# Optimization experiments

Hardware: AMD Instinct MI355X
Metric: run time of the kernel (lower is better)

Reference implementation:

```python
import jax, jax.numpy as jnp
import numpy as np

NUM_HEADS = 16
HEAD_DIM = 64
INNER = NUM_HEADS * HEAD_DIM  # 1024
QUERY_DIM = 1024
CONTEXT_DIM = 768
SCALE = HEAD_DIM ** -0.5


def setup_inputs() -> dict:
    key = jax.random.key(0)
    ks = jax.random.split(key, 6)
    B, NQ, NKV = 8, 1024, 2048
    query = jax.random.normal(ks[0], (B, NQ, QUERY_DIM), dtype=jnp.float32)
    context = jax.random.normal(ks[1], (B, NKV, CONTEXT_DIM), dtype=jnp.float32)
    # weights stored as [in, out] (transpose of torch Linear), math-equivalent
    w_q = jax.random.normal(ks[2], (QUERY_DIM, INNER), dtype=jnp.float32) * (QUERY_DIM ** -0.5)
    w_kv = jax.random.normal(ks[3], (CONTEXT_DIM, 2 * INNER), dtype=jnp.float32) * (CONTEXT_DIM ** -0.5)
    w_out = jax.random.normal(ks[4], (INNER, QUERY_DIM), dtype=jnp.float32) * (INNER ** -0.5)
    b_out = jax.random.normal(ks[5], (QUERY_DIM,), dtype=jnp.float32) * 0.01
    return {"query": query, "context": context, "w_q": w_q, "w_kv": w_kv,
            "w_out": w_out, "b_out": b_out}


def reference(query, context, w_q, w_kv, w_out, b_out):
    B, NQ, _ = query.shape
    NKV = context.shape[1]
    q = query @ w_q                              # [B, NQ, INNER]
    kv = context @ w_kv                          # [B, NKV, 2*INNER]
    k, v = jnp.split(kv, 2, axis=-1)
    # reshape to [B, H, N, D]
    q = q.reshape(B, NQ, NUM_HEADS, HEAD_DIM).transpose(0, 2, 1, 3)
    k = k.reshape(B, NKV, NUM_HEADS, HEAD_DIM).transpose(0, 2, 1, 3)
    v = v.reshape(B, NKV, NUM_HEADS, HEAD_DIM).transpose(0, 2, 1, 3)
    scores = jnp.einsum('bhqd,bhkd->bhqk', q, k) * SCALE
    attn = jax.nn.softmax(scores, axis=-1)
    out = jnp.einsum('bhqk,bhkd->bhqd', attn, v)  # [B, H, NQ, D]
    out = out.transpose(0, 2, 1, 3).reshape(B, NQ, INNER)
    return out @ w_out + b_out
```

## Files before the change

kernel.cpp:

```cpp
#include <hip/hip_runtime.h>
#include <stdint.h>

typedef __bf16 bf16_t;
typedef bf16_t bf16x8 __attribute__((ext_vector_type(8)));
typedef float f32x4 __attribute__((ext_vector_type(4)));
typedef float f32x16 __attribute__((ext_vector_type(16)));

__device__ __forceinline__ unsigned short f2bf(float x) {
    unsigned u = __builtin_bit_cast(unsigned, x);
    u = (u + 0x7FFFu + ((u >> 16) & 1u)) >> 16;
    return (unsigned short)u;
}

__device__ __forceinline__ unsigned pk_bf16(float lo, float hi) {
    unsigned u0 = __builtin_bit_cast(unsigned, lo) + 0x8000u;
    unsigned u1 = __builtin_bit_cast(unsigned, hi) + 0x8000u;
    return __builtin_amdgcn_perm(u1, u0, 0x07060302u);
}

__device__ __forceinline__ void async_load16(const void* g, void* lds) {
    auto* gp = reinterpret_cast<const __attribute__((address_space(1))) uint32_t*>(
        reinterpret_cast<uintptr_t>(g));
    auto* lp = reinterpret_cast<__attribute__((address_space(3))) uint32_t*>(
        reinterpret_cast<uintptr_t>(lds));
    __builtin_amdgcn_global_load_lds(gp, lp, 16, 0, 0);
}

__global__ __launch_bounds__(256) void cast_f32_bf16(const float* __restrict__ src,
                                                     unsigned short* __restrict__ dst,
                                                     int n8) {
    int i = blockIdx.x * 256 + threadIdx.x;
    if (i >= n8) return;
    const float4* s4 = (const float4*)src;
    float4 a = s4[i * 2], b = s4[i * 2 + 1];
    uint4 o;
    o.x = (unsigned)f2bf(a.x) | ((unsigned)f2bf(a.y) << 16);
    o.y = (unsigned)f2bf(a.z) | ((unsigned)f2bf(a.w) << 16);
    o.z = (unsigned)f2bf(b.x) | ((unsigned)f2bf(b.y) << 16);
    o.w = (unsigned)f2bf(b.z) | ((unsigned)f2bf(b.w) << 16);
    ((uint4*)dst)[i] = o;
}

__global__ __launch_bounds__(256) void transcast(const float* __restrict__ src,
                                                 unsigned short* __restrict__ dst,
                                                 int K, int N, float scale) {
    __shared__ float tile[32][33];
    int x = threadIdx.x, y = threadIdx.y;
    int c0 = blockIdx.x * 32, r0 = blockIdx.y * 32;
    #pragma unroll
    for (int i = 0; i < 32; i += 8)
        tile[y + i][x] = src[(size_t)(r0 + y + i) * N + c0 + x];
    __syncthreads();
    #pragma unroll
    for (int i = 0; i < 32; i += 8)
        dst[(size_t)(c0 + y + i) * K + r0 + x] = f2bf(tile[x][y + i] * scale);
}

template <int EPI>
__global__ __launch_bounds__(256) void gemm_bt(const unsigned short* __restrict__ A,
                                               const unsigned short* __restrict__ Bt,
                                               void* __restrict__ Cout,
                                               const float* __restrict__ bias,
                                               int K, int N, int nkt) {
    __shared__ __align__(16) unsigned short lA[128 * 64];
    __shared__ __align__(16) unsigned short lB[128 * 64];
    const int tid = threadIdx.x;
    const int w = tid >> 6, l = tid & 63;
    const int wm = w >> 1, wn = w & 1;
    const int row0 = blockIdx.y * 128, col0 = blockIdx.x * 128;
    const int lrow = l & 15, lq = l >> 4;
    const int srow = l >> 3;
    const int scol = ((l & 7) ^ srow) * 8;

    f32x4 acc[4][4];
    #pragma unroll
    for (int i = 0; i < 4; ++i)
        #pragma unroll
        for (int j = 0; j < 4; ++j) acc[i][j] = (f32x4)0.f;

    for (int kt = 0; kt < nkt; ++kt) {
        const int k0 = kt * 64;
        __syncthreads();
        #pragma unroll
        for (int q = 0; q < 4; ++q) {
            int r = (w * 4 + q) * 8 + srow;
            async_load16(A + (size_t)(row0 + r) * K + k0 + scol,
                         (char*)lA + (w * 4 + q) * 1024);
            async_load16(Bt + (size_t)(col0 + r) * K + k0 + scol,
                         (char*)lB + (w * 4 + q) * 1024);
        }
        __syncthreads();
        #pragma unroll
        for (int kc = 0; kc < 2; ++kc) {
            const int pc = ((kc * 4 + lq) ^ (lrow & 7)) * 16;
            bf16x8 af[4], bfr[4];
            #pragma unroll
            for (int i = 0; i < 4; ++i)
                af[i] = *(const bf16x8*)((const char*)lA + (wm * 64 + i * 16 + lrow) * 128 + pc);
            #pragma unroll
            for (int j = 0; j < 4; ++j)
                bfr[j] = *(const bf16x8*)((const char*)lB + (wn * 64 + j * 16 + lrow) * 128 + pc);
            #pragma unroll
            for (int i = 0; i < 4; ++i)
                #pragma unroll
                for (int j = 0; j < 4; ++j)
                    acc[i][j] = __builtin_amdgcn_mfma_f32_16x16x32_bf16(af[i], bfr[j],
                                                                        acc[i][j], 0, 0, 0);
        }
    }
    #pragma unroll
    for (int i = 0; i < 4; ++i) {
        const int grow0 = row0 + wm * 64 + i * 16 + lq * 4;
        #pragma unroll
        for (int j = 0; j < 4; ++j) {
            const int gcol = col0 + wn * 64 + j * 16 + lrow;
            #pragma unroll
            for (int r = 0; r < 4; ++r) {
                float v = acc[i][j][r];
                int grow = grow0 + r;
                if (EPI == 0) {
                    ((unsigned short*)Cout)[(size_t)grow * N + gcol] = f2bf(v);
                } else {
                    ((float*)Cout)[(size_t)grow * N + gcol] = v + bias[gcol];
                }
            }
        }
    }
}

__global__ __launch_bounds__(256, 2) void gemm_kv(const unsigned short* __restrict__ A,
                                                  const unsigned short* __restrict__ Bt,
                                                  unsigned short* __restrict__ Kb,
                                                  unsigned short* __restrict__ Vt) {
    __shared__ __align__(16) unsigned short lA[256 * 64];
    __shared__ __align__(16) unsigned short lB[128 * 64];
    const int tid = threadIdx.x;
    const int w = tid >> 6, l = tid & 63;
    const int wm = w >> 1, wn = w & 1;
    const int row0 = blockIdx.y * 256, col0 = blockIdx.x * 128;
    const int r32 = l & 31, hw = l >> 5;
    const int srow = l >> 3, scol = ((l & 7) ^ srow) * 8;

    f32x16 acc[4][2];
    #pragma unroll
    for (int mi = 0; mi < 4; ++mi)
        #pragma unroll
        for (int ni = 0; ni < 2; ++ni) acc[mi][ni] = (f32x16)0.f;

    const unsigned short* ga = A + (size_t)(row0 + w * 8 + srow) * 768 + scol;
    const unsigned short* gb = Bt + (size_t)(col0 + w * 8 + srow) * 768 + scol;
    char* lAw = (char*)lA + (w * 8) * 128;
    char* lBw = (char*)lB + (w * 8) * 128;
    const char* lap = (const char*)lA + (wm * 128 + r32) * 128;
    const char* lbp = (const char*)lB + (wn * 64 + r32) * 128;
    const int r7 = r32 & 7;

    for (int kt = 0; kt < 12; ++kt) {
        __syncthreads();
        #pragma unroll
        for (int q = 0; q < 8; ++q)
            async_load16(ga + (size_t)q * 32 * 768, lAw + q * 32 * 128);
        #pragma unroll
        for (int q = 0; q < 4; ++q)
            async_load16(gb + (size_t)q * 32 * 768, lBw + q * 32 * 128);
        ga += 64;
        gb += 64;
        __syncthreads();
        #pragma unroll
        for (int ks = 0; ks < 4; ++ks) {
            const int off = ((ks * 2 + hw) ^ r7) * 16;
            bf16x8 af[4], bfr[2];
            #pragma unroll
            for (int mi = 0; mi < 4; ++mi)
                af[mi] = *(const bf16x8*)(lap + mi * 32 * 128 + off);
            #pragma unroll
            for (int ni = 0; ni < 2; ++ni)
                bfr[ni] = *(const bf16x8*)(lbp + ni * 32 * 128 + off);
            #pragma unroll
            for (int mi = 0; mi < 4; ++mi)
                #pragma unroll
                for (int ni = 0; ni < 2; ++ni)
                    acc[mi][ni] = __builtin_amdgcn_mfma_f32_32x32x16_bf16(af[mi], bfr[ni],
                                                                          acc[mi][ni], 0, 0, 0);
        }
    }

    if (col0 < 1024) {
        unsigned short* kp = Kb + (size_t)(row0 + wm * 128) * 1024 + col0 + wn * 64 + r32;
        #pragma unroll
        for (int mi = 0; mi < 4; ++mi)
            #pragma unroll
            for (int ni = 0; ni < 2; ++ni)
                #pragma unroll
                for (int reg = 0; reg < 16; ++reg) {
                    int rr = mi * 32 + (reg & 3) + 8 * (reg >> 2) + 4 * hw;
                    kp[(size_t)rr * 1024 + ni * 32] = f2bf(acc[mi][ni][reg]);
                }
    } else {
        const int bb = row0 >> 11;
        const int keybase = (row0 & 2047) + wm * 128 + 4 * hw;
        const int fvbase = col0 - 1024 + wn * 64 + r32;
        unsigned short* vp = Vt + ((size_t)bb * 1024 + fvbase) * 2048 + keybase;
        #pragma unroll
        for (int mi = 0; mi < 4; ++mi)
            #pragma unroll
            for (int ni = 0; ni < 2; ++ni)
                #pragma unroll
                for (int g = 0; g < 4; ++g) {
                    uint2 pk2;
                    pk2.x = pk_bf16(acc[mi][ni][g * 4 + 0], acc[mi][ni][g * 4 + 1]);
                    pk2.y = pk_bf16(acc[mi][ni][g * 4 + 2], acc[mi][ni][g * 4 + 3]);
                    *(uint2*)(vp + (size_t)(ni * 32) * 2048 + mi * 32 + g * 8) = pk2;
                }
    }
}

__global__ __launch_bounds__(256, 4) void attn_fwd(const unsigned short* __restrict__ qb,
                                                   const unsigned short* __restrict__ kb,
                                                   const unsigned short* __restrict__ vt,
                                                   unsigned short* __restrict__ ob) {
    constexpr int PSTR = 72;
    __shared__ __align__(16) unsigned short lK[64 * 64];
    __shared__ __align__(16) unsigned short lV[64 * 64];
    __shared__ __align__(16) unsigned short lP[4][32 * PSTR];
    const int tid = threadIdx.x;
    const int w = tid >> 6, l = tid & 63;
    const int b = blockIdx.z, h = blockIdx.y, q0 = blockIdx.x * 128;
    const int lrow = l & 15, lq = l >> 4;
    const int srow = l >> 3, scol = ((l & 7) ^ (srow & 7)) * 8;

    bf16x8 bq[2][2];
    #pragma unroll
    for (int qs = 0; qs < 2; ++qs)
        #pragma unroll
        for (int kc = 0; kc < 2; ++kc) {
            int row = b * 1024 + q0 + w * 32 + qs * 16 + lrow;
            int col = h * 64 + kc * 32 + lq * 8;
            bq[qs][kc] = *(const bf16x8*)(qb + (size_t)row * 1024 + col);
        }

    f32x4 ot[2][4];
    f32x4 lsv[2];
    #pragma unroll
    for (int qs = 0; qs < 2; ++qs) {
        #pragma unroll
        for (int dt = 0; dt < 4; ++dt) ot[qs][dt] = (f32x4)0.f;
        lsv[qs] = (f32x4)0.f;
    }

    const char* kp0 = (const char*)lK + lrow * 128 + ((lq ^ (lrow & 7)) * 16);
    const char* kp1 = (const char*)lK + lrow * 128 + (((4 + lq) ^ (lrow & 7)) * 16);
    const char* vp0 = (const char*)lV + lrow * 128 + ((lq ^ (lrow & 7)) * 16);
    const char* vp1 = (const char*)lV + lrow * 128 + (((4 + lq) ^ (lrow & 7)) * 16);
    char* pw[2];
    const char* pr[2];
    #pragma unroll
    for (int qs = 0; qs < 2; ++qs) {
        pw[qs] = (char*)&lP[w][(qs * 16 + lrow) * PSTR + 4 * lq];
        pr[qs] = (const char*)&lP[w][(qs * 16 + lrow) * PSTR + 8 * lq];
    }

    const unsigned short* gkp = kb + (size_t)b * 2048 * 1024 + h * 64 +
                                (size_t)(w * 8 + srow) * 1024 + scol;
    const unsigned short* gvp = vt + (size_t)(b * 1024 + h * 64) * 2048 +
                                (size_t)(w * 8 + srow) * 2048 + scol;
    char* lKw0 = (char*)lK + (w * 8) * 128;
    char* lKw1 = (char*)lK + (32 + w * 8) * 128;
    char* lVw0 = (char*)lV + (w * 8) * 128;
    char* lVw1 = (char*)lV + (32 + w * 8) * 128;

    for (int it = 0; it < 32; ++it) {
        __syncthreads();
        async_load16(gkp, lKw0);
        async_load16(gkp + 32 * 1024, lKw1);
        async_load16(gvp, lVw0);
        async_load16(gvp + 32 * 2048, lVw1);
        gkp += 64 * 1024;
        gvp += 64;
        __syncthreads();

        f32x4 st[2][4];
        #pragma unroll
        for (int mt = 0; mt < 4; ++mt) {
            bf16x8 ka0 = *(const bf16x8*)(kp0 + mt * 2048);
            bf16x8 ka1 = *(const bf16x8*)(kp1 + mt * 2048);
            #pragma unroll
            for (int qs = 0; qs < 2; ++qs) {
                f32x4 c = (f32x4)0.f;
                c = __builtin_amdgcn_mfma_f32_16x16x32_bf16(ka0, bq[qs][0], c, 0, 0, 0);
                c = __builtin_amdgcn_mfma_f32_16x16x32_bf16(ka1, bq[qs][1], c, 0, 0, 0);
                st[qs][mt] = c;
            }
        }

        #pragma unroll
        for (int qs = 0; qs < 2; ++qs) {
            #pragma unroll
            for (int mt = 0; mt < 4; ++mt)
                #pragma unroll
                for (int r = 0; r < 4; ++r)
                    st[qs][mt][r] = __builtin_amdgcn_exp2f(st[qs][mt][r]);
            lsv[qs] += (st[qs][0] + st[qs][1]) + (st[qs][2] + st[qs][3]);
            #pragma unroll
            for (int mt = 0; mt < 4; ++mt) {
                uint2 pk;
                pk.x = pk_bf16(st[qs][mt][0], st[qs][mt][1]);
                pk.y = pk_bf16(st[qs][mt][2], st[qs][mt][3]);
                *(uint2*)(pw[qs] + 32 * mt) = pk;
            }
        }

        bf16x8 pb[2][2];
        #pragma unroll
        for (int qs = 0; qs < 2; ++qs)
            #pragma unroll
            for (int kcg = 0; kcg < 2; ++kcg)
                pb[qs][kcg] = *(const bf16x8*)(pr[qs] + 64 * kcg);

        #pragma unroll
        for (int dt = 0; dt < 4; ++dt) {
            bf16x8 va0 = *(const bf16x8*)(vp0 + dt * 2048);
            bf16x8 va1 = *(const bf16x8*)(vp1 + dt * 2048);
            #pragma unroll
            for (int qs = 0; qs < 2; ++qs) {
                ot[qs][dt] = __builtin_amdgcn_mfma_f32_16x16x32_bf16(va0, pb[qs][0], ot[qs][dt], 0, 0, 0);
                ot[qs][dt] = __builtin_amdgcn_mfma_f32_16x16x32_bf16(va1, pb[qs][1], ot[qs][dt], 0, 0, 0);
            }
        }
    }

    #pragma unroll
    for (int qs = 0; qs < 2; ++qs) {
        float rs = (lsv[qs][0] + lsv[qs][1]) + (lsv[qs][2] + lsv[qs][3]);
        rs += __shfl_xor(rs, 16);
        rs += __shfl_xor(rs, 32);
        float inv = 1.f / rs;
        size_t grow = (size_t)(b * 1024 + q0 + w * 32 + qs * 16 + lrow);
        unsigned short* op = ob + grow * 1024 + h * 64 + 4 * lq;
        #pragma unroll
        for (int dt = 0; dt < 4; ++dt) {
            uint2 pk;
            pk.x = pk_bf16(ot[qs][dt][0] * inv, ot[qs][dt][1] * inv);
            pk.y = pk_bf16(ot[qs][dt][2] * inv, ot[qs][dt][3] * inv);
            *(uint2*)(op + 16 * dt) = pk;
        }
    }
}

extern "C" void kernel_launch(void* const* d_in, const int* in_sizes, int n_in,
                              void* d_out, int out_size, void* d_ws, size_t ws_size,
                              hipStream_t stream) {
    const float* query   = (const float*)d_in[0];
    const float* context = (const float*)d_in[1];
    const float* w_q     = (const float*)d_in[2];
    const float* w_kv    = (const float*)d_in[3];
    const float* w_out   = (const float*)d_in[4];
    const float* b_out   = (const float*)d_in[5];
    float* out = (float*)d_out;

    char* p = (char*)d_ws;
    unsigned short* qin   = (unsigned short*)p; p += (size_t)8192 * 1024 * 2;
    unsigned short* cin   = (unsigned short*)p; p += (size_t)16384 * 768 * 2;
    unsigned short* wqT   = (unsigned short*)p; p += (size_t)1024 * 1024 * 2;
    unsigned short* wkvT  = (unsigned short*)p; p += (size_t)2048 * 768 * 2;
    unsigned short* woutT = (unsigned short*)p; p += (size_t)1024 * 1024 * 2;
    unsigned short* qproj = (unsigned short*)p; p += (size_t)8192 * 1024 * 2;
    unsigned short* kbuf  = (unsigned short*)p; p += (size_t)16384 * 1024 * 2;
    unsigned short* vT    = (unsigned short*)p; p += (size_t)16384 * 1024 * 2;
    unsigned short* obuf  = (unsigned short*)p; p += (size_t)8192 * 1024 * 2;

    const float qscale = 0.125f * 1.44269504088896f;

    cast_f32_bf16<<<8388608 / 8 / 256, 256, 0, stream>>>(query, qin, 8388608 / 8);
    cast_f32_bf16<<<12582912 / 8 / 256, 256, 0, stream>>>(context, cin, 12582912 / 8);
    transcast<<<dim3(32, 32), dim3(32, 8), 0, stream>>>(w_q, wqT, 1024, 1024, qscale);
    transcast<<<dim3(64, 24), dim3(32, 8), 0, stream>>>(w_kv, wkvT, 768, 2048, 1.0f);
    transcast<<<dim3(32, 32), dim3(32, 8), 0, stream>>>(w_out, woutT, 1024, 1024, 1.0f);
    gemm_bt<0><<<dim3(8, 64), 256, 0, stream>>>(qin, wqT, qproj, nullptr, 1024, 1024, 16);
    gemm_kv<<<dim3(16, 64), 256, 0, stream>>>(cin, wkvT, kbuf, vT);
    attn_fwd<<<dim3(8, 16, 8), 256, 0, stream>>>(qproj, kbuf, vT, obuf);
    gemm_bt<2><<<dim3(8, 64), 256, 0, stream>>>(obuf, woutT, out, b_out, 1024, 1024, 16);
}
```

Measured before the change: 364.2 us.

## Double query rows per attention block and compute row sums via MFMA

```diff
diff --git a/kernel.cpp b/kernel.cpp
--- a/kernel.cpp
+++ b/kernel.cpp
@@ -215,7 +215,7 @@
     }
 }
 
-__global__ __launch_bounds__(256, 4) void attn_fwd(const unsigned short* __restrict__ qb,
+__global__ __launch_bounds__(256, 2) void attn_fwd(const unsigned short* __restrict__ qb,
                                                    const unsigned short* __restrict__ kb,
                                                    const unsigned short* __restrict__ vt,
                                                    unsigned short* __restrict__ ob) {
@@ -225,28 +225,33 @@
     __shared__ __align__(16) unsigned short lP[4][32 * PSTR];
     const int tid = threadIdx.x;
     const int w = tid >> 6, l = tid & 63;
-    const int b = blockIdx.z, h = blockIdx.y, q0 = blockIdx.x * 128;
+    const int bh = blockIdx.x;
+    const int b = bh >> 4, h = bh & 15;
+    const int q0 = blockIdx.y * 256;
     const int lrow = l & 15, lq = l >> 4;
     const int srow = l >> 3, scol = ((l & 7) ^ (srow & 7)) * 8;
 
-    bf16x8 bq[2][2];
-    #pragma unroll
-    for (int qs = 0; qs < 2; ++qs)
+    bf16x8 bq[4][2];
+    #pragma unroll
+    for (int qs = 0; qs < 4; ++qs)
         #pragma unroll
         for (int kc = 0; kc < 2; ++kc) {
-            int row = b * 1024 + q0 + w * 32 + qs * 16 + lrow;
+            int row = b * 1024 + q0 + w * 64 + qs * 16 + lrow;
             int col = h * 64 + kc * 32 + lq * 8;
             bq[qs][kc] = *(const bf16x8*)(qb + (size_t)row * 1024 + col);
         }
 
-    f32x4 ot[2][4];
-    f32x4 lsv[2];
-    #pragma unroll
-    for (int qs = 0; qs < 2; ++qs) {
+    f32x4 ot[4][4];
+    f32x4 lfr[4];
+    #pragma unroll
+    for (int qs = 0; qs < 4; ++qs) {
         #pragma unroll
         for (int dt = 0; dt < 4; ++dt) ot[qs][dt] = (f32x4)0.f;
-        lsv[qs] = (f32x4)0.f;
-    }
+        lfr[qs] = (f32x4)0.f;
+    }
+    bf16x8 one8;
+    #pragma unroll
+    for (int i = 0; i < 8; ++i) one8[i] = (bf16_t)1.0f;
 
     const char* kp0 = (const char*)lK + lrow * 128 + ((lq ^ (lrow & 7)) * 16);
     const char* kp1 = (const char*)lK + lrow * 128 + (((4 + lq) ^ (lrow & 7)) * 16);
@@ -255,9 +260,9 @@
     char* pw[2];
     const char* pr[2];
     #pragma unroll
-    for (int qs = 0; qs < 2; ++qs) {
-        pw[qs] = (char*)&lP[w][(qs * 16 + lrow) * PSTR + 4 * lq];
-        pr[qs] = (const char*)&lP[w][(qs * 16 + lrow) * PSTR + 8 * lq];
+    for (int u = 0; u < 2; ++u) {
+        pw[u] = (char*)&lP[w][(u * 16 + lrow) * PSTR + 4 * lq];
+        pr[u] = (const char*)&lP[w][(u * 16 + lrow) * PSTR + 8 * lq];
     }
 
     const unsigned short* gkp = kb + (size_t)b * 2048 * 1024 + h * 64 +
@@ -279,63 +284,69 @@
         gvp += 64;
         __syncthreads();
 
-        f32x4 st[2][4];
+        bf16x8 ka[4][2], va[4][2];
         #pragma unroll
         for (int mt = 0; mt < 4; ++mt) {
-            bf16x8 ka0 = *(const bf16x8*)(kp0 + mt * 2048);
-            bf16x8 ka1 = *(const bf16x8*)(kp1 + mt * 2048);
-            #pragma unroll
-            for (int qs = 0; qs < 2; ++qs) {
-                f32x4 c = (f32x4)0.f;
-                c = __builtin_amdgcn_mfma_f32_16x16x32_bf16(ka0, bq[qs][0], c, 0, 0, 0);
-                c = __builtin_amdgcn_mfma_f32_16x16x32_bf16(ka1, bq[qs][1], c, 0, 0, 0);
-                st[qs][mt] = c;
+            ka[mt][0] = *(const bf16x8*)(kp0 + mt * 2048);
+            ka[mt][1] = *(const bf16x8*)(kp1 + mt * 2048);
+        }
+        #pragma unroll
+        for (int dt = 0; dt < 4; ++dt) {
+            va[dt][0] = *(const bf16x8*)(vp0 + dt * 2048);
+            va[dt][1] = *(const bf16x8*)(vp1 + dt * 2048);
+        }
+
+        #pragma unroll
+        for (int p = 0; p < 2; ++p) {
+            f32x4 st[2][4];
+            #pragma unroll
+            for (int u = 0; u < 2; ++u) {
+                const int qs = 2 * p + u;
+                #pragma unroll
+                for (int mt = 0; mt < 4; ++mt) {
+                    f32x4 c = (f32x4)0.f;
+                    c = __builtin_amdgcn_mfma_f32_16x16x32_bf16(ka[mt][0], bq[qs][0], c, 0, 0, 0);
+                    c = __builtin_amdgcn_mfma_f32_16x16x32_bf16(ka[mt][1], bq[qs][1], c, 0, 0, 0);
+                    st[u][mt] = c;
+                }
             }
-        }
-
-        #pragma unroll
-        for (int qs = 0; qs < 2; ++qs) {
-            #pragma unroll
-            for (int mt = 0; mt < 4; ++mt)
-                #pragma unroll
-                for (int r = 0; r < 4; ++r)
-                    st[qs][mt][r] = __builtin_amdgcn_exp2f(st[qs][mt][r]);
-            lsv[qs] += (st[qs][0] + st[qs][1]) + (st[qs][2] + st[qs][3]);
-            #pragma unroll
-            for (int mt = 0; mt < 4; ++mt) {
-                uint2 pk;
-                pk.x = pk_bf16(st[qs][mt][0], st[qs][mt][1]);
-                pk.y = pk_bf16(st[qs][mt][2], st[qs][mt][3]);
-                *(uint2*)(pw[qs] + 32 * mt) = pk;
+            #pragma unroll
+            for (int u = 0; u < 2; ++u) {
+                #pragma unroll
+                for (int mt = 0; mt < 4; ++mt) {
+                    #pragma unroll
+                    for (int r = 0; r < 4; ++r)
+                        st[u][mt][r] = __builtin_amdgcn_exp2f(st[u][mt][r]);
+                    uint2 pk;
+                    pk.x = pk_bf16(st[u][mt][0], st[u][mt][1]);
+                    pk.y = pk_bf16(st[u][mt][2], st[u][mt][3]);
+                    *(uint2*)(pw[u] + 32 * mt) = pk;
+                }
             }
-        }
-
-        bf16x8 pb[2][2];
-        #pragma unroll
-        for (int qs = 0; qs < 2; ++qs)
-            #pragma unroll
-            for (int kcg = 0; kcg < 2; ++kcg)
-                pb[qs][kcg] = *(const bf16x8*)(pr[qs] + 64 * kcg);
-
-        #pragma unroll
-        for (int dt = 0; dt < 4; ++dt) {
-            bf16x8 va0 = *(const bf16x8*)(vp0 + dt * 2048);
-            bf16x8 va1 = *(const bf16x8*)(vp1 + dt * 2048);
-            #pragma unroll
-            for (int qs = 0; qs < 2; ++qs) {
-                ot[qs][dt] = __builtin_amdgcn_mfma_f32_16x16x32_bf16(va0, pb[qs][0], ot[qs][dt], 0, 0, 0);
-                ot[qs][dt] = __builtin_amdgcn_mfma_f32_16x16x32_bf16(va1, pb[qs][1], ot[qs][dt], 0, 0, 0);
+            bf16x8 pb[2][2];
+            #pragma unroll
+            for (int u = 0; u < 2; ++u)
+                #pragma unroll
+                for (int kcg = 0; kcg < 2; ++kcg)
+                    pb[u][kcg] = *(const bf16x8*)(pr[u] + 64 * kcg);
+            #pragma unroll
+            for (int u = 0; u < 2; ++u) {
+                const int qs = 2 * p + u;
+                lfr[qs] = __builtin_amdgcn_mfma_f32_16x16x32_bf16(one8, pb[u][0], lfr[qs], 0, 0, 0);
+                lfr[qs] = __builtin_amdgcn_mfma_f32_16x16x32_bf16(one8, pb[u][1], lfr[qs], 0, 0, 0);
+                #pragma unroll
+                for (int dt = 0; dt < 4; ++dt) {
+                    ot[qs][dt] = __builtin_amdgcn_mfma_f32_16x16x32_bf16(va[dt][0], pb[u][0], ot[qs][dt], 0, 0, 0);
+                    ot[qs][dt] = __builtin_amdgcn_mfma_f32_16x16x32_bf16(va[dt][1], pb[u][1], ot[qs][dt], 0, 0, 0);
+                }
             }
         }
     }
 
     #pragma unroll
-    for (int qs = 0; qs < 2; ++qs) {
-        float rs = (lsv[qs][0] + lsv[qs][1]) + (lsv[qs][2] + lsv[qs][3]);
-        rs += __shfl_xor(rs, 16);
-        rs += __shfl_xor(rs, 32);
-        float inv = 1.f / rs;
-        size_t grow = (size_t)(b * 1024 + q0 + w * 32 + qs * 16 + lrow);
+    for (int qs = 0; qs < 4; ++qs) {
+        float inv = 1.f / lfr[qs][0];
+        size_t grow = (size_t)(b * 1024 + q0 + w * 64 + qs * 16 + lrow);
         unsigned short* op = ob + grow * 1024 + h * 64 + 4 * lq;
         #pragma unroll
         for (int dt = 0; dt < 4; ++dt) {
@@ -378,6 +389,6 @@
     transcast<<<dim3(32, 32), dim3(32, 8), 0, stream>>>(w_out, woutT, 1024, 1024, 1.0f);
     gemm_bt<0><<<dim3(8, 64), 256, 0, stream>>>(qin, wqT, qproj, nullptr, 1024, 1024, 16);
     gemm_kv<<<dim3(16, 64), 256, 0, stream>>>(cin, wkvT, kbuf, vT);
-    attn_fwd<<<dim3(8, 16, 8), 256, 0, stream>>>(qproj, kbuf, vT, obuf);
+    attn_fwd<<<dim3(128, 4), 256, 0, stream>>>(qproj, kbuf, vT, obuf);
     gemm_bt<2><<<dim3(8, 64), 256, 0, stream>>>(obuf, woutT, out, b_out, 1024, 1024, 16);
 }
```

New measurement: 358.3 us. About the same (-1.6%).
